# Optimization experiments

Measured on AMD Instinct MI355X. Metric: run time of the kernel, lower is better.

## Reference

```python
import jax, jax.numpy as jnp
import numpy as np

EPS = 1e-5
B, S, P = 2, 512, 4096
TD, SD, H, ED = 512, 384, 8, 32
HD = TD // H


def _ln(x, g, b):
    m = jnp.mean(x, axis=-1, keepdims=True)
    v = jnp.var(x, axis=-1, keepdims=True)
    return (x - m) * jax.lax.rsqrt(v + EPS) * g + b


def setup_inputs() -> dict:
    key = jax.random.key(0)
    ks = iter(jax.random.split(key, 24))

    def lin(din, dout):
        W = jax.random.normal(next(ks), (din, dout), jnp.float32) / np.sqrt(din)
        b = jnp.zeros((dout,), jnp.float32)
        return W, b

    Wq, bq = lin(TD, TD)
    Wk, bk = lin(SD, TD)
    Wv, bv = lin(SD, TD)
    Wo, bo = lin(TD, TD)
    W1, b1 = lin(TD, 4 * TD)
    W2, b2 = lin(4 * TD, TD)
    edge_emb = jax.random.normal(next(ks), (H, ED), jnp.float32)
    ep_w = jax.random.normal(next(ks), (ED,), jnp.float32) / np.sqrt(ED)
    ep_b = jnp.zeros((), jnp.float32)

    return dict(
        text_features=jax.random.normal(next(ks), (B, S, TD), jnp.float32),
        shape_features=jax.random.normal(next(ks), (B, P, SD), jnp.float32),
        tn_g=jnp.ones((TD,), jnp.float32), tn_b=jnp.zeros((TD,), jnp.float32),
        sn_g=jnp.ones((SD,), jnp.float32), sn_b=jnp.zeros((SD,), jnp.float32),
        Wq=Wq, bq=bq, Wk=Wk, bk=bk, Wv=Wv, bv=bv,
        edge_emb=edge_emb, ep_w=ep_w, ep_b=ep_b,
        Wo=Wo, bo=bo,
        on_g=jnp.ones((TD,), jnp.float32), on_b=jnp.zeros((TD,), jnp.float32),
        W1=W1, b1=b1, W2=W2, b2=b2,
        fn_g=jnp.ones((TD,), jnp.float32), fn_b=jnp.zeros((TD,), jnp.float32),
    )


def reference(text_features, shape_features, tn_g, tn_b, sn_g, sn_b,
              Wq, bq, Wk, bk, Wv, bv, edge_emb, ep_w, ep_b, Wo, bo,
              on_g, on_b, W1, b1, W2, b2, fn_g, fn_b):
    b, n, _ = text_features.shape
    tn = _ln(text_features, tn_g, tn_b)
    sn = _ln(shape_features, sn_g, sn_b)
    residual = text_features

    # [b, h, n, d] projections
    q = (tn @ Wq + bq).reshape(b, n, H, HD).transpose(0, 2, 1, 3)
    k = (sn @ Wk + bk).reshape(b, -1, H, HD).transpose(0, 2, 1, 3)
    v = (sn @ Wv + bv).reshape(b, -1, H, HD).transpose(0, 2, 1, 3)

    scale = HD ** -0.5
    base_attn = jnp.einsum('bhid,bhjd->bhij', q, k) * scale  # [b,h,n,p]

    # edge_attn[:,h] = base_attn[:,h,:,:,None] * edge_emb[h]; then Linear(ED,1)+LeakyReLU.
    # Algebraically: score = leaky_relu(base_attn * (edge_emb @ ep_w) + ep_b)
    s = edge_emb @ ep_w  # [H] per-head scalar
    edge_scores = jax.nn.leaky_relu(base_attn * s[None, :, None, None] + ep_b, 0.2)

    attn = jax.nn.softmax(base_attn + edge_scores, axis=-1)
    out = jnp.einsum('bhij,bhjd->bhid', attn, v)
    out = out.transpose(0, 2, 1, 3).reshape(b, n, TD)
    out = out @ Wo + bo
    out = _ln(residual + out, on_g, on_b)

    ffn = jax.nn.gelu(out @ W1 + b1, approximate=False) @ W2 + b2
    out = _ln(out + ffn, fn_g, fn_b)
    return out, attn
```

## Files before the change

kernel.cpp:

```cpp
#include <hip/hip_runtime.h>
#include <math.h>

#define B_  2
#define S_  512
#define P_  4096
#define TD_ 512
#define SD_ 384
#define H_  8
#define HD_ 64
#define FF_ 2048

typedef _Float16 half8 __attribute__((ext_vector_type(8)));
typedef _Float16 half4 __attribute__((ext_vector_type(4)));
typedef float floatx4 __attribute__((ext_vector_type(4)));

__device__ __forceinline__ float2 block_sum2(float a, float b) {
    for (int off = 32; off > 0; off >>= 1) {
        a += __shfl_down(a, off);
        b += __shfl_down(b, off);
    }
    __shared__ float sa[8], sb[8];
    int w = threadIdx.x >> 6;
    if ((threadIdx.x & 63) == 0) { sa[w] = a; sb[w] = b; }
    __syncthreads();
    int nw = blockDim.x >> 6;
    float ta = 0.f, tb = 0.f;
    for (int i = 0; i < nw; ++i) { ta += sa[i]; tb += sb[i]; }
    __syncthreads();
    return make_float2(ta, tb);
}

__global__ __launch_bounds__(256) void prep_kernel(
    const float* __restrict__ s0p, const float* __restrict__ s1p,
    const float* __restrict__ s2p, const float* __restrict__ s3p,
    const float* __restrict__ s4p, const float* __restrict__ s5p,
    _Float16* __restrict__ d0p, _Float16* __restrict__ d1p,
    _Float16* __restrict__ d2p, _Float16* __restrict__ d3p,
    _Float16* __restrict__ d4p, _Float16* __restrict__ d5p,
    const float* __restrict__ text, const float* __restrict__ shape,
    const float* __restrict__ tn_g, const float* __restrict__ tn_b,
    const float* __restrict__ sn_g, const float* __restrict__ sn_b,
    _Float16* __restrict__ tn_h, _Float16* __restrict__ sn_h)
{
    __shared__ float ts[32][33];
    int id = blockIdx.x;
    int tid = threadIdx.x;
    if (id < 2944) {
        const float* src; _Float16* dst; int K, N, t, nlog;
        if (id < 256)       { src=s0p; dst=d0p; K=512;  N=512;  t=id;       nlog=4; }
        else if (id < 448)  { src=s1p; dst=d1p; K=384;  N=512;  t=id-256;   nlog=4; }
        else if (id < 640)  { src=s2p; dst=d2p; K=384;  N=512;  t=id-448;   nlog=4; }
        else if (id < 896)  { src=s3p; dst=d3p; K=512;  N=512;  t=id-640;   nlog=4; }
        else if (id < 1920) { src=s4p; dst=d4p; K=512;  N=2048; t=id-896;   nlog=6; }
        else                { src=s5p; dst=d5p; K=2048; N=512;  t=id-1920;  nlog=4; }
        int n0 = (t & ((1 << nlog) - 1)) << 5;
        int k0 = (t >> nlog) << 5;
#pragma unroll
        for (int i = 0; i < 4; ++i) {
            int e = i * 256 + tid;
            int kk = e >> 5, nn = e & 31;
            ts[kk][nn] = src[(size_t)(k0 + kk) * N + n0 + nn];
        }
        __syncthreads();
#pragma unroll
        for (int i = 0; i < 4; ++i) {
            int e = i * 256 + tid;
            int nn = e >> 5, kk = e & 31;
            dst[(size_t)(n0 + nn) * K + k0 + kk] = (_Float16)ts[kk][nn];
        }
        return;
    }
    int row = id - 2944;
    const float* xr; const float* g; const float* be; _Float16* yr; int D;
    if (row < 1024) {
        D = 512; xr = text + (size_t)row * 512; g = tn_g; be = tn_b;
        yr = tn_h + (size_t)row * 512;
    } else {
        int r2 = row - 1024;
        D = 384; xr = shape + (size_t)r2 * 384; g = sn_g; be = sn_b;
        yr = sn_h + (size_t)r2 * 384;
    }
    float s = 0.f, s2 = 0.f;
    for (int i = tid; i < D; i += 256) {
        float v = xr[i]; s += v; s2 += v * v;
    }
    float2 r = block_sum2(s, s2);
    float mean = r.x / (float)D;
    float var  = r.y / (float)D - mean * mean;
    float rstd = rsqrtf(var + 1e-5f);
    for (int i = tid; i < D; i += 256)
        yr[i] = (_Float16)((xr[i] - mean) * rstd * g[i] + be[i]);
}

__global__ __launch_bounds__(256) void ln_add_kernel(
    const float* __restrict__ a, const float* __restrict__ c, int np, int cstride,
    const float* __restrict__ g, const float* __restrict__ be,
    float* __restrict__ yf, _Float16* __restrict__ yh)
{
    int row = blockIdx.x;
    int i0 = threadIdx.x, i1 = threadIdx.x + 256;
    const float* ar = a + (size_t)row * 512;
    const float* cr = c + (size_t)row * 512;
    float v0 = ar[i0], v1 = ar[i1];
    for (int t = 0; t < np; ++t) {
        v0 += cr[(size_t)t * cstride + i0];
        v1 += cr[(size_t)t * cstride + i1];
    }
    float2 rd = block_sum2(v0 + v1, v0 * v0 + v1 * v1);
    float mean = rd.x / 512.f;
    float var  = rd.y / 512.f - mean * mean;
    float rstd = rsqrtf(var + 1e-5f);
    float o0 = (v0 - mean) * rstd * g[i0] + be[i0];
    float o1 = (v1 - mean) * rstd * g[i1] + be[i1];
    if (yf) { yf[(size_t)row * 512 + i0] = o0; yf[(size_t)row * 512 + i1] = o1; }
    if (yh) { yh[(size_t)row * 512 + i0] = (_Float16)o0; yh[(size_t)row * 512 + i1] = (_Float16)o1; }
}

template<int ACT, int OUTF, int OUTH, int SPLITK>
__global__ __launch_bounds__(256) void gemm_f16_kernel(
    const _Float16* __restrict__ A, const _Float16* __restrict__ Bt,
    const float* __restrict__ bias, float* __restrict__ Cf,
    _Float16* __restrict__ Ch, int M, int N, int K)
{
    __shared__ _Float16 As[128 * 40];
    __shared__ _Float16 Bs[128 * 40];
    int tid = threadIdx.x;
    int bm = blockIdx.y * 128, bn = blockIdx.x * 128;
    int wave = tid >> 6, lane = tid & 63, quad = lane >> 4, r = lane & 15;
    int mh = (wave & 1) * 64, nh = (wave >> 1) * 64;

    floatx4 acc[4][4];
    floatx4 zz = {0.f, 0.f, 0.f, 0.f};
#pragma unroll
    for (int i = 0; i < 4; ++i)
#pragma unroll
        for (int j = 0; j < 4; ++j) acc[i][j] = zz;

    int srow = tid >> 2;
    int sko  = (tid & 3) * 8;

    int ksplit = (SPLITK > 1) ? blockIdx.z : 0;
    int kbeg = ksplit * (K / SPLITK);
    int kend = kbeg + K / SPLITK;

    const _Float16* Ap0 = A  + (size_t)(bm + srow) * K + sko;
    const _Float16* Ap1 = A  + (size_t)(bm + srow + 64) * K + sko;
    const _Float16* Bp0 = Bt + (size_t)(bn + srow) * K + sko;
    const _Float16* Bp1 = Bt + (size_t)(bn + srow + 64) * K + sko;

    half8 ra0 = *(const half8*)(Ap0 + kbeg);
    half8 ra1 = *(const half8*)(Ap1 + kbeg);
    half8 rb0 = *(const half8*)(Bp0 + kbeg);
    half8 rb1 = *(const half8*)(Bp1 + kbeg);

    for (int k0 = kbeg; k0 < kend; k0 += 32) {
        *(half8*)&As[srow * 40 + sko]        = ra0;
        *(half8*)&As[(srow + 64) * 40 + sko] = ra1;
        *(half8*)&Bs[srow * 40 + sko]        = rb0;
        *(half8*)&Bs[(srow + 64) * 40 + sko] = rb1;
        __syncthreads();
        if (k0 + 32 < kend) {
            ra0 = *(const half8*)(Ap0 + k0 + 32);
            ra1 = *(const half8*)(Ap1 + k0 + 32);
            rb0 = *(const half8*)(Bp0 + k0 + 32);
            rb1 = *(const half8*)(Bp1 + k0 + 32);
        }
        half8 af[4], bf[4];
#pragma unroll
        for (int t = 0; t < 4; ++t) {
            af[t] = *(const half8*)&As[(mh + t * 16 + r) * 40 + quad * 8];
            bf[t] = *(const half8*)&Bs[(nh + t * 16 + r) * 40 + quad * 8];
        }
#pragma unroll
        for (int i = 0; i < 4; ++i)
#pragma unroll
            for (int j = 0; j < 4; ++j)
                acc[i][j] = __builtin_amdgcn_mfma_f32_16x16x32_f16(af[i], bf[j], acc[i][j], 0, 0, 0);
        __syncthreads();
    }

#pragma unroll
    for (int j = 0; j < 4; ++j) {
        int col = bn + nh + j * 16 + r;
        float bv = (SPLITK == 1 || ksplit == 0) ? bias[col] : 0.f;
#pragma unroll
        for (int i = 0; i < 4; ++i) {
#pragma unroll
            for (int g = 0; g < 4; ++g) {
                int row = bm + mh + i * 16 + quad * 4 + g;
                float v = acc[i][j][g] + bv;
                if (ACT) v = 0.5f * v * (1.0f + erff(v * 0.70710678118654752f));
                if (OUTF) Cf[(size_t)ksplit * M * N + (size_t)row * N + col] = v;
                if (OUTH) Ch[(size_t)row * N + col] = (_Float16)v;
            }
        }
    }
}

__global__ __launch_bounds__(512) void qkv_gemm_kernel(
    const _Float16* __restrict__ tn, const _Float16* __restrict__ sn,
    const _Float16* __restrict__ Wqt, const _Float16* __restrict__ Wkt,
    const _Float16* __restrict__ Wvt,
    const float* __restrict__ bq, const float* __restrict__ bk,
    const float* __restrict__ bv,
    _Float16* __restrict__ Qh, _Float16* __restrict__ Kh, _Float16* __restrict__ Vth)
{
    __shared__ _Float16 As[256 * 40];
    __shared__ _Float16 Bs[128 * 40];
    int by = blockIdx.y;
    const _Float16* A; const _Float16* Bt; const float* bias; _Float16* out;
    int K, bm, vt;
    if (by < 4)       { A = tn; Bt = Wqt; bias = bq; K = 512; bm = by * 256;        vt = 0; out = Qh;  }
    else if (by < 36) { A = sn; Bt = Wkt; bias = bk; K = 384; bm = (by - 4) * 256;  vt = 0; out = Kh;  }
    else              { A = sn; Bt = Wvt; bias = bv; K = 384; bm = (by - 36) * 256; vt = 1; out = Vth; }
    int bn = blockIdx.x * 128;
    int tid = threadIdx.x;
    int wave = tid >> 6, lane = tid & 63, quad = lane >> 4, r = lane & 15;
    int mh = (wave >> 1) * 64, nh = (wave & 1) * 64;

    floatx4 acc[4][4];
    floatx4 zz = {0.f, 0.f, 0.f, 0.f};
#pragma unroll
    for (int i = 0; i < 4; ++i)
#pragma unroll
        for (int j = 0; j < 4; ++j) acc[i][j] = zz;

    int arow = tid >> 2, ako = (tid & 3) * 8;
    const _Float16* ApA0 = A  + (size_t)(bm + arow) * K + ako;
    const _Float16* ApA1 = A  + (size_t)(bm + arow + 128) * K + ako;
    const _Float16* BpB  = Bt + (size_t)(bn + arow) * K + ako;

    half8 ra0 = *(const half8*)(ApA0);
    half8 ra1 = *(const half8*)(ApA1);
    half8 rb  = *(const half8*)(BpB);

    for (int k0 = 0; k0 < K; k0 += 32) {
        *(half8*)&As[arow * 40 + ako]         = ra0;
        *(half8*)&As[(arow + 128) * 40 + ako] = ra1;
        *(half8*)&Bs[arow * 40 + ako]         = rb;
        __syncthreads();
        if (k0 + 32 < K) {
            ra0 = *(const half8*)(ApA0 + k0 + 32);
            ra1 = *(const half8*)(ApA1 + k0 + 32);
            rb  = *(const half8*)(BpB  + k0 + 32);
        }
        half8 af[4], bf[4];
#pragma unroll
        for (int t = 0; t < 4; ++t) {
            af[t] = *(const half8*)&As[(mh + t * 16 + r) * 40 + quad * 8];
            bf[t] = *(const half8*)&Bs[(nh + t * 16 + r) * 40 + quad * 8];
        }
#pragma unroll
        for (int i = 0; i < 4; ++i)
#pragma unroll
            for (int j = 0; j < 4; ++j)
                acc[i][j] = __builtin_amdgcn_mfma_f32_16x16x32_f16(af[i], bf[j], acc[i][j], 0, 0, 0);
        __syncthreads();
    }

#pragma unroll
    for (int j = 0; j < 4; ++j) {
        int col = bn + nh + j * 16 + r;
        float bvv = bias[col];
#pragma unroll
        for (int i = 0; i < 4; ++i) {
#pragma unroll
            for (int g = 0; g < 4; ++g) {
                int row = bm + mh + i * 16 + quad * 4 + g;
                float v = acc[i][j][g] + bvv;
                if (!vt) {
                    out[(size_t)row * 512 + col] = (_Float16)v;
                } else {
                    int bb = row >> 12, pp = row & 4095;
                    int hh = col >> 6,  dd = col & 63;
                    out[((size_t)((bb * 8 + hh) * 64 + dd)) * 4096 + pp] = (_Float16)v;
                }
            }
        }
    }
}

__global__ __launch_bounds__(256) void score_stats_kernel(
    const _Float16* __restrict__ Qh, const _Float16* __restrict__ Kh,
    const float* __restrict__ edge_emb, const float* __restrict__ ep_w,
    const float* __restrict__ ep_b, float2* __restrict__ part)
{
    __shared__ _Float16 Qs[128 * 72];
    __shared__ _Float16 Ks[128 * 72];
    __shared__ float mred[2][128];
    __shared__ float sred[2][128];
    int p0 = blockIdx.x * 128, s0 = blockIdx.y * 128;
    int bh = blockIdx.z, h = bh & 7, b = bh >> 3;
    int tid = threadIdx.x;
    int wave = tid >> 6, lane = tid & 63, quad = lane >> 4, r = lane & 15;
    int mh = (wave & 1) * 64, nh = (wave >> 1) * 64;

#pragma unroll
    for (int i = 0; i < 4; ++i) {
        int row = i * 32 + (tid >> 3);
        int ko  = (tid & 7) * 8;
        *(half8*)&Qs[row * 72 + ko] = *(const half8*)(Qh + (size_t)(b * S_ + s0 + row) * TD_ + h * HD_ + ko);
        *(half8*)&Ks[row * 72 + ko] = *(const half8*)(Kh + (size_t)(b * P_ + p0 + row) * TD_ + h * HD_ + ko);
    }
    float s_h = 0.f;
#pragma unroll
    for (int e = 0; e < 32; ++e) s_h += edge_emb[h * 32 + e] * ep_w[e];
    float epbv = ep_b[0];
    __syncthreads();

    floatx4 acc[4][4];
    floatx4 zz = {0.f, 0.f, 0.f, 0.f};
#pragma unroll
    for (int i = 0; i < 4; ++i)
#pragma unroll
        for (int j = 0; j < 4; ++j) acc[i][j] = zz;

#pragma unroll
    for (int c = 0; c < 2; ++c) {
        half8 af[4], bf[4];
#pragma unroll
        for (int t = 0; t < 4; ++t) {
            af[t] = *(const half8*)&Qs[(mh + t * 16 + r) * 72 + c * 32 + quad * 8];
            bf[t] = *(const half8*)&Ks[(nh + t * 16 + r) * 72 + c * 32 + quad * 8];
        }
#pragma unroll
        for (int i = 0; i < 4; ++i)
#pragma unroll
            for (int j = 0; j < 4; ++j)
                acc[i][j] = __builtin_amdgcn_mfma_f32_16x16x32_f16(af[i], bf[j], acc[i][j], 0, 0, 0);
    }

    const float scale = 0.125f;
#pragma unroll
    for (int i = 0; i < 4; ++i)
#pragma unroll
        for (int j = 0; j < 4; ++j)
#pragma unroll
            for (int g = 0; g < 4; ++g) {
                float base = acc[i][j][g] * scale;
                float t = fmaf(base, s_h, epbv);
                float e = (t >= 0.f) ? t : 0.2f * t;
                acc[i][j][g] = base + e;
            }

    float mv[16], sv[16];
#pragma unroll
    for (int i = 0; i < 4; ++i)
#pragma unroll
        for (int g = 0; g < 4; ++g)
            mv[i * 4 + g] = fmaxf(fmaxf(acc[i][0][g], acc[i][1][g]),
                                  fmaxf(acc[i][2][g], acc[i][3][g]));
#pragma unroll
    for (int mask = 1; mask <= 8; mask <<= 1)
#pragma unroll
        for (int t = 0; t < 16; ++t)
            mv[t] = fmaxf(mv[t], __shfl_xor(mv[t], mask));
#pragma unroll
    for (int i = 0; i < 4; ++i)
#pragma unroll
        for (int g = 0; g < 4; ++g) {
            float s = 0.f;
#pragma unroll
            for (int j = 0; j < 4; ++j) s += __expf(acc[i][j][g] - mv[i * 4 + g]);
            sv[i * 4 + g] = s;
        }
#pragma unroll
    for (int mask = 1; mask <= 8; mask <<= 1)
#pragma unroll
        for (int t = 0; t < 16; ++t)
            sv[t] += __shfl_xor(sv[t], mask);

    if (r == 0) {
#pragma unroll
        for (int i = 0; i < 4; ++i)
#pragma unroll
            for (int g = 0; g < 4; ++g) {
                int row = mh + i * 16 + quad * 4 + g;
                mred[wave >> 1][row] = mv[i * 4 + g];
                sred[wave >> 1][row] = sv[i * 4 + g];
            }
    }
    __syncthreads();
    if (tid < 128) {
        float m0 = mred[0][tid], m1 = mred[1][tid];
        float m = fmaxf(m0, m1);
        float s = sred[0][tid] * __expf(m0 - m) + sred[1][tid] * __expf(m1 - m);
        part[(size_t)blockIdx.x * (B_ * H_ * S_) + (size_t)bh * S_ + s0 + tid] = make_float2(m, s);
    }
}

__global__ __launch_bounds__(256) void attn_pv_kernel(
    const _Float16* __restrict__ Qh, const _Float16* __restrict__ Kh,
    const _Float16* __restrict__ Vt,
    const float* __restrict__ edge_emb, const float* __restrict__ ep_w,
    const float* __restrict__ ep_b, const float2* __restrict__ part,
    float* __restrict__ attn, float* __restrict__ ctx_part)
{
    __shared__ _Float16 Qs[32 * 72];
    __shared__ _Float16 Ks[128 * 72];
    __shared__ _Float16 Vs[64 * 136];
    __shared__ _Float16 As[32 * 136];
    __shared__ float2 ms_sh[32];

    int s0 = blockIdx.x * 32;
    int split = blockIdx.y;
    int bh = blockIdx.z, h = bh & 7, b = bh >> 3;
    int tid = threadIdx.x;
    int wave = tid >> 6, lane = tid & 63, quad = lane >> 4, r = lane & 15;

    {
        int row = tid >> 3, ko = (tid & 7) * 8;
        *(half8*)&Qs[row * 72 + ko] =
            *(const half8*)(Qh + (size_t)(b * S_ + s0 + row) * TD_ + h * HD_ + ko);
    }
    if (tid < 32) {
        int base = bh * S_ + s0 + tid;
        float2 v = part[base];
        float m = v.x, l = v.y;
#pragma unroll
        for (int t = 1; t < 32; ++t) {
            float2 p = part[(size_t)t * (B_ * H_ * S_) + base];
            float nm = fmaxf(m, p.x);
            l = l * __expf(m - nm) + p.y * __expf(p.x - nm);
            m = nm;
        }
        ms_sh[tid] = make_float2(m, 1.0f / l);
    }

    float s_h = 0.f;
#pragma unroll
    for (int e = 0; e < 32; ++e) s_h += edge_emb[h * 32 + e] * ep_w[e];
    float epbv = ep_b[0];

    const _Float16* Kbase = Kh + (size_t)b * P_ * TD_ + h * HD_;
    const _Float16* Vbase = Vt + (size_t)bh * 64 * P_;

    int pg0 = split * 512;
    half8 rk[4], rv[4];
#pragma unroll
    for (int ii = 0; ii < 4; ++ii) {
        int e = ii * 256 + tid;
        rk[ii] = *(const half8*)(Kbase + (size_t)(pg0 + (e >> 3)) * TD_ + (e & 7) * 8);
        rv[ii] = *(const half8*)(Vbase + (size_t)(e >> 4) * P_ + pg0 + (e & 15) * 8);
    }

    floatx4 zz = {0.f, 0.f, 0.f, 0.f};
    floatx4 accpv[2];
    accpv[0] = zz; accpv[1] = zz;
    const float scale = 0.125f;

    for (int c = 0; c < 4; ++c) {
        int pg = pg0 + c * 128;
#pragma unroll
        for (int ii = 0; ii < 4; ++ii) {
            int e = ii * 256 + tid;
            *(half8*)&Ks[(e >> 3) * 72 + (e & 7) * 8]  = rk[ii];
            *(half8*)&Vs[(e >> 4) * 136 + (e & 15) * 8] = rv[ii];
        }
        __syncthreads();
        if (c < 3) {
            int pn = pg + 128;
#pragma unroll
            for (int ii = 0; ii < 4; ++ii) {
                int e = ii * 256 + tid;
                rk[ii] = *(const half8*)(Kbase + (size_t)(pn + (e >> 3)) * TD_ + (e & 7) * 8);
                rv[ii] = *(const half8*)(Vbase + (size_t)(e >> 4) * P_ + pn + (e & 15) * 8);
            }
        }

        floatx4 accs[2][2];
        accs[0][0] = zz; accs[0][1] = zz; accs[1][0] = zz; accs[1][1] = zz;
#pragma unroll
        for (int c2 = 0; c2 < 2; ++c2) {
            half8 aq[2], bk2[2];
#pragma unroll
            for (int i = 0; i < 2; ++i)
                aq[i] = *(const half8*)&Qs[(i * 16 + r) * 72 + c2 * 32 + quad * 8];
#pragma unroll
            for (int j = 0; j < 2; ++j)
                bk2[j] = *(const half8*)&Ks[(wave * 32 + j * 16 + r) * 72 + c2 * 32 + quad * 8];
#pragma unroll
            for (int i = 0; i < 2; ++i)
#pragma unroll
                for (int j = 0; j < 2; ++j)
                    accs[i][j] = __builtin_amdgcn_mfma_f32_16x16x32_f16(aq[i], bk2[j], accs[i][j], 0, 0, 0);
        }

#pragma unroll
        for (int i = 0; i < 2; ++i)
#pragma unroll
            for (int j = 0; j < 2; ++j) {
                int colp = wave * 32 + j * 16 + r;
#pragma unroll
                for (int g = 0; g < 4; ++g) {
                    int srow = i * 16 + quad * 4 + g;
                    float base = accs[i][j][g] * scale;
                    float t = fmaf(base, s_h, epbv);
                    float e = (t >= 0.f) ? t : 0.2f * t;
                    float z = base + e;
                    float2 ms = ms_sh[srow];
                    float p = __expf(z - ms.x) * ms.y;
                    __builtin_nontemporal_store(p, &attn[((size_t)bh * S_ + s0 + srow) * P_ + pg + colp]);
                    As[srow * 136 + colp] = (_Float16)p;
                }
            }
        __syncthreads();

#pragma unroll
        for (int cc = 0; cc < 4; ++cc) {
            half8 bv = *(const half8*)&Vs[(wave * 16 + r) * 136 + cc * 32 + quad * 8];
#pragma unroll
            for (int i2 = 0; i2 < 2; ++i2) {
                half8 ap = *(const half8*)&As[(i2 * 16 + r) * 136 + cc * 32 + quad * 8];
                accpv[i2] = __builtin_amdgcn_mfma_f32_16x16x32_f16(ap, bv, accpv[i2], 0, 0, 0);
            }
        }
        __syncthreads();
    }

    float* dst = ctx_part + (size_t)split * (1024 * 512);
#pragma unroll
    for (int i2 = 0; i2 < 2; ++i2)
#pragma unroll
        for (int g = 0; g < 4; ++g) {
            int srow = s0 + i2 * 16 + quad * 4 + g;
            int d = wave * 16 + r;
            dst[(size_t)(b * S_ + srow) * TD_ + h * HD_ + d] = accpv[i2][g];
        }
}

__global__ __launch_bounds__(256) void sumcast_kernel(
    const float4* __restrict__ src, _Float16* __restrict__ dst, int n4)
{
    int i = blockIdx.x * 256 + threadIdx.x;
    if (i < n4) {
        float4 v = src[i];
#pragma unroll
        for (int t = 1; t < 8; ++t) {
            float4 p = src[i + t * 131072];
            v.x += p.x; v.y += p.y; v.z += p.z; v.w += p.w;
        }
        half4 hv = { (_Float16)v.x, (_Float16)v.y, (_Float16)v.z, (_Float16)v.w };
        *(half4*)&dst[(size_t)i * 4] = hv;
    }
}

extern "C" void kernel_launch(void* const* d_in, const int* in_sizes, int n_in,
                              void* d_out, int out_size, void* d_ws, size_t ws_size,
                              hipStream_t stream) {
    const float* text  = (const float*)d_in[0];
    const float* shape = (const float*)d_in[1];
    const float* tn_g  = (const float*)d_in[2];
    const float* tn_b  = (const float*)d_in[3];
    const float* sn_g  = (const float*)d_in[4];
    const float* sn_b  = (const float*)d_in[5];
    const float* Wq    = (const float*)d_in[6];
    const float* bq    = (const float*)d_in[7];
    const float* Wk    = (const float*)d_in[8];
    const float* bk    = (const float*)d_in[9];
    const float* Wv    = (const float*)d_in[10];
    const float* bv    = (const float*)d_in[11];
    const float* edge  = (const float*)d_in[12];
    const float* epw   = (const float*)d_in[13];
    const float* epb   = (const float*)d_in[14];
    const float* Wo    = (const float*)d_in[15];
    const float* bo    = (const float*)d_in[16];
    const float* on_g  = (const float*)d_in[17];
    const float* on_b  = (const float*)d_in[18];
    const float* W1    = (const float*)d_in[19];
    const float* b1    = (const float*)d_in[20];
    const float* W2    = (const float*)d_in[21];
    const float* b2    = (const float*)d_in[22];
    const float* fn_g  = (const float*)d_in[23];
    const float* fn_b  = (const float*)d_in[24];

    float* out_f  = (float*)d_out;
    float* attn_f = out_f + (size_t)B_ * S_ * TD_;

    char* w = (char*)d_ws;
    _Float16* tn_h   = (_Float16*)w; w += (size_t)1024 * 512 * 2;
    _Float16* sn_h   = (_Float16*)w; w += (size_t)8192 * 384 * 2;
    _Float16* Q_h    = (_Float16*)w; w += (size_t)1024 * 512 * 2;
    _Float16* K_h    = (_Float16*)w; w += (size_t)8192 * 512 * 2;
    _Float16* Vt_h   = (_Float16*)w; w += (size_t)16 * 64 * 4096 * 2;
    _Float16* ctx_h  = (_Float16*)w; w += (size_t)1024 * 512 * 2;
    _Float16* out1_h = (_Float16*)w; w += (size_t)1024 * 512 * 2;
    _Float16* h1_h   = (_Float16*)w; w += (size_t)1024 * 2048 * 2;
    _Float16* Wqt    = (_Float16*)w; w += (size_t)512 * 512 * 2;
    _Float16* Wkt    = (_Float16*)w; w += (size_t)512 * 384 * 2;
    _Float16* Wvt    = (_Float16*)w; w += (size_t)512 * 384 * 2;
    _Float16* Wot    = (_Float16*)w; w += (size_t)512 * 512 * 2;
    _Float16* W1t    = (_Float16*)w; w += (size_t)2048 * 512 * 2;
    _Float16* W2t    = (_Float16*)w; w += (size_t)512 * 2048 * 2;
    float*    out1_f = (float*)w;    w += (size_t)1024 * 512 * 4;
    float*    ctx_part = (float*)w;  w += (size_t)8 * 1024 * 512 * 4;

    float2* part = (float2*)sn_h;

    prep_kernel<<<2944 + 1024 + 8192, 256, 0, stream>>>(
        Wq, Wk, Wv, Wo, W1, W2, Wqt, Wkt, Wvt, Wot, W1t, W2t,
        text, shape, tn_g, tn_b, sn_g, sn_b, tn_h, sn_h);

    qkv_gemm_kernel<<<dim3(4, 68), 512, 0, stream>>>(tn_h, sn_h, Wqt, Wkt, Wvt,
                                                     bq, bk, bv, Q_h, K_h, Vt_h);

    score_stats_kernel<<<dim3(P_ / 128, S_ / 128, B_ * H_), 256, 0, stream>>>(
        Q_h, K_h, edge, epw, epb, part);
    attn_pv_kernel<<<dim3(S_ / 32, 8, B_ * H_), 256, 0, stream>>>(
        Q_h, K_h, Vt_h, edge, epw, epb, part, attn_f, ctx_part);
    sumcast_kernel<<<dim3(512), 256, 0, stream>>>((const float4*)ctx_part, ctx_h, 131072);

    gemm_f16_kernel<0,1,0,4><<<dim3(4, 8, 4), 256, 0, stream>>>(ctx_h, Wot, bo, ctx_part, nullptr, 1024, 512, 512);
    ln_add_kernel<<<B_ * S_, 256, 0, stream>>>(text, ctx_part, 4, 1024 * 512, on_g, on_b, out1_f, out1_h);

    gemm_f16_kernel<1,0,1,1><<<dim3(16, 8), 256, 0, stream>>>(out1_h, W1t, b1, nullptr, h1_h, 1024, 2048, 512);
    gemm_f16_kernel<0,1,0,4><<<dim3(4, 8, 4), 256, 0, stream>>>(h1_h, W2t, b2, ctx_part, nullptr, 1024, 512, 2048);
    ln_add_kernel<<<B_ * S_, 256, 0, stream>>>(out1_f, ctx_part, 4, 1024 * 512, fn_g, fn_b, out_f, nullptr);
}
```

Before: 357.2 us.

## Replace split-K context partials with atomics, vectorize attn stores, remap grid

The attention-PV kernel now accumulates its 8 key-split partial contexts straight into a zeroed fp32 buffer with atomicAdd. This removes the sumcast reduction kernel and its 16 MB partial buffer, and the zeroing is folded into extra blocks of the prep kernel. The Wo GEMM gains an AF32 path that reads the fp32 context and converts it to fp16 while staging tiles into shared memory. Attention probabilities are now written as 128-bit nontemporal stores read back from the fp16 shared tile, so the stored attn output passes through fp16 rounding. The score and PV kernels use a 1D grid remapped so that the 8 blocks in each consecutive group share an s-tile and differ in split or p, to change the cache locality pattern; the atomics add nondeterminism and contention.

```diff
diff --git a/kernel.cpp b/kernel.cpp
--- a/kernel.cpp
+++ b/kernel.cpp
@@ -13,6 +13,13 @@
 typedef _Float16 half8 __attribute__((ext_vector_type(8)));
 typedef _Float16 half4 __attribute__((ext_vector_type(4)));
 typedef float floatx4 __attribute__((ext_vector_type(4)));
+
+__device__ __forceinline__ half8 f4x2_to_h8(float4 a, float4 b) {
+    half8 r;
+    r[0] = (_Float16)a.x; r[1] = (_Float16)a.y; r[2] = (_Float16)a.z; r[3] = (_Float16)a.w;
+    r[4] = (_Float16)b.x; r[5] = (_Float16)b.y; r[6] = (_Float16)b.z; r[7] = (_Float16)b.w;
+    return r;
+}
 
 __device__ __forceinline__ float2 block_sum2(float a, float b) {
     for (int off = 32; off > 0; off >>= 1) {
@@ -40,7 +47,8 @@
     const float* __restrict__ text, const float* __restrict__ shape,
     const float* __restrict__ tn_g, const float* __restrict__ tn_b,
     const float* __restrict__ sn_g, const float* __restrict__ sn_b,
-    _Float16* __restrict__ tn_h, _Float16* __restrict__ sn_h)
+    _Float16* __restrict__ tn_h, _Float16* __restrict__ sn_h,
+    float* __restrict__ ctx_zero)
 {
     __shared__ float ts[32][33];
     int id = blockIdx.x;
@@ -70,6 +78,11 @@
         }
         return;
     }
+    if (id >= 12160) {
+        int i = (id - 12160) * 256 + tid;
+        ((float4*)ctx_zero)[i] = make_float4(0.f, 0.f, 0.f, 0.f);
+        return;
+    }
     int row = id - 2944;
     const float* xr; const float* g; const float* be; _Float16* yr; int D;
     if (row < 1024) {
@@ -116,7 +129,7 @@
     if (yh) { yh[(size_t)row * 512 + i0] = (_Float16)o0; yh[(size_t)row * 512 + i1] = (_Float16)o1; }
 }
 
-template<int ACT, int OUTF, int OUTH, int SPLITK>
+template<int ACT, int OUTF, int OUTH, int SPLITK, int AF32>
 __global__ __launch_bounds__(256) void gemm_f16_kernel(
     const _Float16* __restrict__ A, const _Float16* __restrict__ Bt,
     const float* __restrict__ bias, float* __restrict__ Cf,
@@ -143,25 +156,45 @@
     int kbeg = ksplit * (K / SPLITK);
     int kend = kbeg + K / SPLITK;
 
+    const float*    Af  = (const float*)A;
     const _Float16* Ap0 = A  + (size_t)(bm + srow) * K + sko;
     const _Float16* Ap1 = A  + (size_t)(bm + srow + 64) * K + sko;
+    const float*    Af0 = Af + (size_t)(bm + srow) * K + sko;
+    const float*    Af1 = Af + (size_t)(bm + srow + 64) * K + sko;
     const _Float16* Bp0 = Bt + (size_t)(bn + srow) * K + sko;
     const _Float16* Bp1 = Bt + (size_t)(bn + srow + 64) * K + sko;
 
-    half8 ra0 = *(const half8*)(Ap0 + kbeg);
-    half8 ra1 = *(const half8*)(Ap1 + kbeg);
+    half8 ra0, ra1;
+    float4 fa0l, fa0h, fa1l, fa1h;
+    if (AF32) {
+        fa0l = *(const float4*)(Af0 + kbeg); fa0h = *(const float4*)(Af0 + kbeg + 4);
+        fa1l = *(const float4*)(Af1 + kbeg); fa1h = *(const float4*)(Af1 + kbeg + 4);
+    } else {
+        ra0 = *(const half8*)(Ap0 + kbeg);
+        ra1 = *(const half8*)(Ap1 + kbeg);
+    }
     half8 rb0 = *(const half8*)(Bp0 + kbeg);
     half8 rb1 = *(const half8*)(Bp1 + kbeg);
 
     for (int k0 = kbeg; k0 < kend; k0 += 32) {
-        *(half8*)&As[srow * 40 + sko]        = ra0;
-        *(half8*)&As[(srow + 64) * 40 + sko] = ra1;
+        if (AF32) {
+            *(half8*)&As[srow * 40 + sko]        = f4x2_to_h8(fa0l, fa0h);
+            *(half8*)&As[(srow + 64) * 40 + sko] = f4x2_to_h8(fa1l, fa1h);
+        } else {
+            *(half8*)&As[srow * 40 + sko]        = ra0;
+            *(half8*)&As[(srow + 64) * 40 + sko] = ra1;
+        }
         *(half8*)&Bs[srow * 40 + sko]        = rb0;
         *(half8*)&Bs[(srow + 64) * 40 + sko] = rb1;
         __syncthreads();
         if (k0 + 32 < kend) {
-            ra0 = *(const half8*)(Ap0 + k0 + 32);
-            ra1 = *(const half8*)(Ap1 + k0 + 32);
+            if (AF32) {
+                fa0l = *(const float4*)(Af0 + k0 + 32); fa0h = *(const float4*)(Af0 + k0 + 36);
+                fa1l = *(const float4*)(Af1 + k0 + 32); fa1h = *(const float4*)(Af1 + k0 + 36);
+            } else {
+                ra0 = *(const half8*)(Ap0 + k0 + 32);
+                ra1 = *(const half8*)(Ap1 + k0 + 32);
+            }
             rb0 = *(const half8*)(Bp0 + k0 + 32);
             rb1 = *(const half8*)(Bp1 + k0 + 32);
         }
@@ -289,8 +322,12 @@
     __shared__ _Float16 Ks[128 * 72];
     __shared__ float mred[2][128];
     __shared__ float sred[2][128];
-    int p0 = blockIdx.x * 128, s0 = blockIdx.y * 128;
-    int bh = blockIdx.z, h = bh & 7, b = bh >> 3;
+    int bid = blockIdx.x;
+    int slot = bid & 7, idx = bid >> 3;
+    int g4 = slot + 8 * (idx >> 2);
+    int s0 = (idx & 3) * 128;
+    int p0 = (g4 & 31) * 128;
+    int bh = g4 >> 5, h = bh & 7, b = bh >> 3;
     int tid = threadIdx.x;
     int wave = tid >> 6, lane = tid & 63, quad = lane >> 4, r = lane & 15;
     int mh = (wave & 1) * 64, nh = (wave >> 1) * 64;
@@ -385,7 +422,7 @@
         float m0 = mred[0][tid], m1 = mred[1][tid];
         float m = fmaxf(m0, m1);
         float s = sred[0][tid] * __expf(m0 - m) + sred[1][tid] * __expf(m1 - m);
-        part[(size_t)blockIdx.x * (B_ * H_ * S_) + (size_t)bh * S_ + s0 + tid] = make_float2(m, s);
+        part[(size_t)(p0 >> 7) * (B_ * H_ * S_) + (size_t)bh * S_ + s0 + tid] = make_float2(m, s);
     }
 }
 
@@ -394,7 +431,7 @@
     const _Float16* __restrict__ Vt,
     const float* __restrict__ edge_emb, const float* __restrict__ ep_w,
     const float* __restrict__ ep_b, const float2* __restrict__ part,
-    float* __restrict__ attn, float* __restrict__ ctx_part)
+    float* __restrict__ attn, float* __restrict__ ctx_f32)
 {
     __shared__ _Float16 Qs[32 * 72];
     __shared__ _Float16 Ks[128 * 72];
@@ -402,9 +439,12 @@
     __shared__ _Float16 As[32 * 136];
     __shared__ float2 ms_sh[32];
 
-    int s0 = blockIdx.x * 32;
-    int split = blockIdx.y;
-    int bh = blockIdx.z, h = bh & 7, b = bh >> 3;
+    int bid = blockIdx.x;
+    int slot = bid & 7, idx = bid >> 3;
+    int g16 = slot + 8 * (idx >> 4);
+    int s0 = (idx & 15) * 32;
+    int split = g16 & 7;
+    int bh = g16 >> 3, h = bh & 7, b = bh >> 3;
     int tid = threadIdx.x;
     int wave = tid >> 6, lane = tid & 63, quad = lane >> 4, r = lane & 15;
 
@@ -500,11 +540,20 @@
                     float z = base + e;
                     float2 ms = ms_sh[srow];
                     float p = __expf(z - ms.x) * ms.y;
-                    __builtin_nontemporal_store(p, &attn[((size_t)bh * S_ + s0 + srow) * P_ + pg + colp]);
                     As[srow * 136 + colp] = (_Float16)p;
                 }
             }
         __syncthreads();
+
+#pragma unroll
+        for (int it = 0; it < 4; ++it) {
+            int e = it * 256 + tid;
+            int row = e >> 5, c4 = (e & 31) * 4;
+            half4 hv = *(const half4*)&As[row * 136 + c4];
+            floatx4 fv = { (float)hv[0], (float)hv[1], (float)hv[2], (float)hv[3] };
+            __builtin_nontemporal_store(fv,
+                (floatx4*)&attn[((size_t)bh * S_ + s0 + row) * P_ + pg + c4]);
+        }
 
 #pragma unroll
         for (int cc = 0; cc < 4; ++cc) {
@@ -518,31 +567,14 @@
         __syncthreads();
     }
 
-    float* dst = ctx_part + (size_t)split * (1024 * 512);
 #pragma unroll
     for (int i2 = 0; i2 < 2; ++i2)
 #pragma unroll
         for (int g = 0; g < 4; ++g) {
             int srow = s0 + i2 * 16 + quad * 4 + g;
             int d = wave * 16 + r;
-            dst[(size_t)(b * S_ + srow) * TD_ + h * HD_ + d] = accpv[i2][g];
-        }
-}
-
-__global__ __launch_bounds__(256) void sumcast_kernel(
-    const float4* __restrict__ src, _Float16* __restrict__ dst, int n4)
-{
-    int i = blockIdx.x * 256 + threadIdx.x;
-    if (i < n4) {
-        float4 v = src[i];
-#pragma unroll
-        for (int t = 1; t < 8; ++t) {
-            float4 p = src[i + t * 131072];
-            v.x += p.x; v.y += p.y; v.z += p.z; v.w += p.w;
-        }
-        half4 hv = { (_Float16)v.x, (_Float16)v.y, (_Float16)v.z, (_Float16)v.w };
-        *(half4*)&dst[(size_t)i * 4] = hv;
-    }
+            atomicAdd(&ctx_f32[(size_t)(b * S_ + srow) * TD_ + h * HD_ + d], accpv[i2][g]);
+        }
 }
 
 extern "C" void kernel_launch(void* const* d_in, const int* in_sizes, int n_in,
@@ -583,7 +615,7 @@
     _Float16* Q_h    = (_Float16*)w; w += (size_t)1024 * 512 * 2;
     _Float16* K_h    = (_Float16*)w; w += (size_t)8192 * 512 * 2;
     _Float16* Vt_h   = (_Float16*)w; w += (size_t)16 * 64 * 4096 * 2;
-    _Float16* ctx_h  = (_Float16*)w; w += (size_t)1024 * 512 * 2;
+    float*    ctx_f32 = (float*)w;   w += (size_t)1024 * 512 * 4;
     _Float16* out1_h = (_Float16*)w; w += (size_t)1024 * 512 * 2;
     _Float16* h1_h   = (_Float16*)w; w += (size_t)1024 * 2048 * 2;
     _Float16* Wqt    = (_Float16*)w; w += (size_t)512 * 512 * 2;
@@ -593,27 +625,25 @@
     _Float16* W1t    = (_Float16*)w; w += (size_t)2048 * 512 * 2;
     _Float16* W2t    = (_Float16*)w; w += (size_t)512 * 2048 * 2;
     float*    out1_f = (float*)w;    w += (size_t)1024 * 512 * 4;
-    float*    ctx_part = (float*)w;  w += (size_t)8 * 1024 * 512 * 4;
+    float*    ctx_part = (float*)w;  w += (size_t)4 * 1024 * 512 * 4;
 
     float2* part = (float2*)sn_h;
 
-    prep_kernel<<<2944 + 1024 + 8192, 256, 0, stream>>>(
+    prep_kernel<<<2944 + 1024 + 8192 + 512, 256, 0, stream>>>(
         Wq, Wk, Wv, Wo, W1, W2, Wqt, Wkt, Wvt, Wot, W1t, W2t,
-        text, shape, tn_g, tn_b, sn_g, sn_b, tn_h, sn_h);
+        text, shape, tn_g, tn_b, sn_g, sn_b, tn_h, sn_h, ctx_f32);
 
     qkv_gemm_kernel<<<dim3(4, 68), 512, 0, stream>>>(tn_h, sn_h, Wqt, Wkt, Wvt,
                                                      bq, bk, bv, Q_h, K_h, Vt_h);
 
-    score_stats_kernel<<<dim3(P_ / 128, S_ / 128, B_ * H_), 256, 0, stream>>>(
-        Q_h, K_h, edge, epw, epb, part);
-    attn_pv_kernel<<<dim3(S_ / 32, 8, B_ * H_), 256, 0, stream>>>(
-        Q_h, K_h, Vt_h, edge, epw, epb, part, attn_f, ctx_part);
-    sumcast_kernel<<<dim3(512), 256, 0, stream>>>((const float4*)ctx_part, ctx_h, 131072);
-
-    gemm_f16_kernel<0,1,0,4><<<dim3(4, 8, 4), 256, 0, stream>>>(ctx_h, Wot, bo, ctx_part, nullptr, 1024, 512, 512);
+    score_stats_kernel<<<2048, 256, 0, stream>>>(Q_h, K_h, edge, epw, epb, part);
+    attn_pv_kernel<<<2048, 256, 0, stream>>>(Q_h, K_h, Vt_h, edge, epw, epb, part, attn_f, ctx_f32);
+
+    gemm_f16_kernel<0,1,0,4,1><<<dim3(4, 8, 4), 256, 0, stream>>>(
+        (const _Float16*)ctx_f32, Wot, bo, ctx_part, nullptr, 1024, 512, 512);
     ln_add_kernel<<<B_ * S_, 256, 0, stream>>>(text, ctx_part, 4, 1024 * 512, on_g, on_b, out1_f, out1_h);
 
-    gemm_f16_kernel<1,0,1,1><<<dim3(16, 8), 256, 0, stream>>>(out1_h, W1t, b1, nullptr, h1_h, 1024, 2048, 512);
-    gemm_f16_kernel<0,1,0,4><<<dim3(4, 8, 4), 256, 0, stream>>>(h1_h, W2t, b2, ctx_part, nullptr, 1024, 512, 2048);
+    gemm_f16_kernel<1,0,1,1,0><<<dim3(16, 8), 256, 0, stream>>>(out1_h, W1t, b1, nullptr, h1_h, 1024, 2048, 512);
+    gemm_f16_kernel<0,1,0,4,0><<<dim3(4, 8, 4), 256, 0, stream>>>(h1_h, W2t, b2, ctx_part, nullptr, 1024, 512, 2048);
     ln_add_kernel<<<B_ * S_, 256, 0, stream>>>(out1_f, ctx_part, 4, 1024 * 512, fn_g, fn_b, out_f, nullptr);
 }
```

Result: faster. 335.2 us (median of 2 runs) (-6.1%).
